# Kernel tuning notes

Hardware: AMD Instinct MI355X
Metric: run time of the kernel (lower is better)

## Reference

```python
import jax, jax.numpy as jnp
import numpy as np
from jax import lax

L, NFEAT, J, S = 200000, 128, 128, 16


def setup_inputs() -> dict:
    key = jax.random.key(0)
    ks = jax.random.split(key, 8)
    X = jax.random.normal(ks[0], (L, NFEAT), dtype=jnp.float32)
    perm_idx = jax.random.randint(ks[1], (L, 2, S), 0, L, dtype=jnp.int64)
    # torch.nn.Linear params: y = x @ W.T + b
    Wh = jax.random.normal(ks[2], (J, NFEAT), dtype=jnp.float32) * 0.05  # h1
    bh = jnp.zeros((J,), jnp.float32)
    Wg = jax.random.normal(ks[3], (J, 2 * J), dtype=jnp.float32) * 0.05  # g1
    bg = jnp.zeros((J,), jnp.float32)
    Wf = jax.random.normal(ks[4], (1, J), dtype=jnp.float32) * 0.05      # final1
    bf = jnp.zeros((1,), jnp.float32)
    return {"X": X, "perm_idx": perm_idx, "Wh": Wh, "bh": bh,
            "Wg": Wg, "bg": bg, "Wf": Wf, "bf": bf}


def reference(X, perm_idx, Wh, bh, Wg, bg, Wf, bf):
    # forward_recursive_vec with neighbor_subset_limit=2.
    # h(x) = relu(h1(x)) depends only on the row of X, so compute once and gather.
    Hmat = jax.nn.relu(X @ Wh.T + bh)                  # (L, J)
    Jdim = Wh.shape[0]
    Wg0, Wg1 = Wg[:, :Jdim], Wg[:, Jdim:]              # split of concat input
    n_samples = perm_idx.shape[-1]
    idxs = jnp.moveaxis(perm_idx, -1, 0)               # (S, L, 2)

    def body(acc, idx):
        # g(cat(h(X[perm0]), h(X[perm1]))) = relu(H[p0] @ Wg0.T + H[p1] @ Wg1.T + bg)
        h0 = Hmat[idx[:, 0]]                           # (L, J) irregular gather
        h1 = Hmat[idx[:, 1]]                           # (L, J) irregular gather
        g = jax.nn.relu(h0 @ Wg0.T + h1 @ Wg1.T + bg)
        return acc + g, None

    acc, _ = lax.scan(body, jnp.zeros_like(Hmat), idxs)
    E = jax.nn.relu(acc / n_samples)                   # E = relu(fk(X, 2))
    # temp = cat(h(X), E); E = g(temp)
    E = jax.nn.relu(Hmat @ Wg0.T + E @ Wg1.T + bg)
    # final(E): plain Linear(J,1), no sigmoid on this path
    return E @ Wf.T + bf                               # (L, 1)
```

## Files before the change

### kernel.cpp

```cpp
#include <hip/hip_runtime.h>

typedef unsigned short u16;
typedef unsigned char u8;
typedef unsigned int u32;
typedef __attribute__((ext_vector_type(8))) short short8;
typedef __attribute__((ext_vector_type(4))) short short4v;
typedef __attribute__((ext_vector_type(4))) float f32x4;
typedef __attribute__((ext_vector_type(2))) float f32x2;
typedef __attribute__((ext_vector_type(4))) u32 u32x4;

#define L_ROWS 200000
#define TM 64
#define LDP 136
#define NWH 16384
#define NWG 32768

__device__ __forceinline__ float b2f(u16 u) {
  union { u32 i; float f; } v; v.i = ((u32)u) << 16; return v.f;
}
__device__ __forceinline__ u16 f2b(float f) {
  union { float fv; u32 i; } v; v.fv = f;
  return (u16)((v.i + 0x7fffu + ((v.i >> 16) & 1u)) >> 16);
}
__device__ __forceinline__ u32 pk4_fp8(float f0, float f1, float f2, float f3) {
  u32 w = __builtin_amdgcn_cvt_pk_fp8_f32(f0, f1, 0, false);
  w = __builtin_amdgcn_cvt_pk_fp8_f32(f2, f3, w, true);
  return w;
}

__global__ __launch_bounds__(256) void kW(const float* __restrict__ Wh,
                                          const float* __restrict__ Wg,
                                          u16* __restrict__ WB) {
  int i = blockIdx.x * 256 + threadIdx.x;
  if (i < NWH) WB[i] = f2b(Wh[i]);
  else WB[i] = f2b(Wg[i - NWH]);
}

__global__ __launch_bounds__(256) void kA(const float* X,
                                          const float* bh,
                                          const u16* __restrict__ WB,
                                          u16* U0b, int strideB,
                                          u8* F0, u8* F1, int strideF) {
  __shared__ u16 tile[TM][LDP];
  const int b = blockIdx.x, t = threadIdx.x;
  const int wave = t >> 6, lane = t & 63;
  const int ln = lane & 15, quad = lane >> 4;
  const u16* WhB = WB;
  const u16* WgB = WB + NWH;

  {
    const float* src = X + (size_t)b * TM * 128;
#pragma unroll
    for (int i = 0; i < 8; i++) {
      int e = t * 4 + i * 1024;
      float4 v = *(const float4*)(src + e);
      u16 pk[4] = { f2b(v.x), f2b(v.y), f2b(v.z), f2b(v.w) };
      *(short4v*)&tile[e >> 7][e & 127] = *(const short4v*)pk;
    }
  }

  __syncthreads();

  f32x4 acc1[4][2] = {};
#pragma unroll
  for (int ks = 0; ks < 4; ks++) {
    short8 bf1[2];
#pragma unroll
    for (int nt = 0; nt < 2; nt++) {
      int n = wave * 32 + nt * 16 + ln;
      bf1[nt] = *(const short8*)(WhB + n * 128 + ks * 32 + quad * 8);
    }
    short8 af[4];
#pragma unroll
    for (int mt = 0; mt < 4; mt++) af[mt] = *(const short8*)&tile[mt * 16 + ln][ks * 32 + quad * 8];
#pragma unroll
    for (int mt = 0; mt < 4; mt++)
#pragma unroll
      for (int nt = 0; nt < 2; nt++)
        acc1[mt][nt] = __builtin_amdgcn_mfma_f32_16x16x32_bf16(af[mt], bf1[nt], acc1[mt][nt], 0, 0, 0);
  }

  __syncthreads();

#pragma unroll
  for (int nt = 0; nt < 2; nt++) {
    int n = wave * 32 + nt * 16 + ln;
    float bias = bh[n];
#pragma unroll
    for (int r = 0; r < 4; r++)
#pragma unroll
      for (int mt = 0; mt < 4; mt++)
        tile[mt * 16 + quad * 4 + r][n] = f2b(fmaxf(acc1[mt][nt][r] + bias, 0.f));
  }

  __syncthreads();

  f32x4 acc2[4][4] = {};
#pragma unroll
  for (int ks = 0; ks < 4; ks++) {
    short8 bf2[4];
#pragma unroll
    for (int nt = 0; nt < 4; nt++) {
      int n = wave * 64 + nt * 16 + ln;
      const u16* base = (n < 128) ? (WgB + n * 256) : (WgB + (n - 128) * 256 + 128);
      bf2[nt] = *(const short8*)(base + ks * 32 + quad * 8);
    }
    short8 af[4];
#pragma unroll
    for (int mt = 0; mt < 4; mt++) af[mt] = *(const short8*)&tile[mt * 16 + ln][ks * 32 + quad * 8];
#pragma unroll
    for (int mt = 0; mt < 4; mt++)
#pragma unroll
      for (int nt = 0; nt < 4; nt++)
        acc2[mt][nt] = __builtin_amdgcn_mfma_f32_16x16x32_bf16(af[mt], bf2[nt], acc2[mt][nt], 0, 0, 0);
  }

  __syncthreads();

  if (wave < 2) {
#pragma unroll
    for (int nt = 0; nt < 4; nt++) {
      int n = wave * 64 + nt * 16 + ln;
#pragma unroll
      for (int mt = 0; mt < 4; mt++)
#pragma unroll
        for (int r = 0; r < 4; r++)
          tile[mt * 16 + quad * 4 + r][n] = f2b(acc2[mt][nt][r]);
    }
  }
  __syncthreads();
  {
    const int rr = t >> 2, cs = (t & 3) * 32;
    const size_t row = (size_t)b * TM + rr;
    u16* dstB = U0b + row * strideB + cs;
    u8* dstF = F0 + row * strideF + cs;
    u32 wpk[8];
#pragma unroll
    for (int c = 0; c < 4; c++) {
      short8 v = *(const short8*)&tile[rr][cs + c * 8];
      *(short8*)(dstB + c * 8) = v;
      wpk[c * 2 + 0] = pk4_fp8(b2f((u16)v[0]), b2f((u16)v[1]), b2f((u16)v[2]), b2f((u16)v[3]));
      wpk[c * 2 + 1] = pk4_fp8(b2f((u16)v[4]), b2f((u16)v[5]), b2f((u16)v[6]), b2f((u16)v[7]));
    }
    *(u32x4*)dstF = u32x4{wpk[0], wpk[1], wpk[2], wpk[3]};
    *(u32x4*)(dstF + 16) = u32x4{wpk[4], wpk[5], wpk[6], wpk[7]};
  }
  __syncthreads();

  if (wave >= 2) {
#pragma unroll
    for (int nt = 0; nt < 4; nt++) {
      int n = wave * 64 + nt * 16 + ln - 128;
#pragma unroll
      for (int mt = 0; mt < 4; mt++)
#pragma unroll
        for (int r = 0; r < 4; r++)
          tile[mt * 16 + quad * 4 + r][n] = f2b(acc2[mt][nt][r]);
    }
  }
  __syncthreads();
  {
    const int rr = t >> 2, cs = (t & 3) * 32;
    const size_t row = (size_t)b * TM + rr;
    u8* dstF = F1 + row * strideF + cs;
    u32 wpk[8];
#pragma unroll
    for (int c = 0; c < 4; c++) {
      short8 v = *(const short8*)&tile[rr][cs + c * 8];
      wpk[c * 2 + 0] = pk4_fp8(b2f((u16)v[0]), b2f((u16)v[1]), b2f((u16)v[2]), b2f((u16)v[3]));
      wpk[c * 2 + 1] = pk4_fp8(b2f((u16)v[4]), b2f((u16)v[5]), b2f((u16)v[6]), b2f((u16)v[7]));
    }
    *(u32x4*)dstF = u32x4{wpk[0], wpk[1], wpk[2], wpk[3]};
    *(u32x4*)(dstF + 16) = u32x4{wpk[4], wpk[5], wpk[6], wpk[7]};
  }
}

__global__ __launch_bounds__(256) void kBC(const int* __restrict__ perm,
                                           const u16* __restrict__ U0b, int strideB,
                                           const u8* __restrict__ F0,
                                           const u8* __restrict__ F1, int strideF,
                                           const u16* __restrict__ WB,
                                           const float* __restrict__ bg,
                                           const float* __restrict__ Wf,
                                           const float* __restrict__ bfs,
                                           float* __restrict__ out) {
  __shared__ u16 Elds[TM][LDP];
  __shared__ float outacc[TM];
  const int b = blockIdx.x, t = threadIdx.x;
  const int wave = t >> 6, lane = t & 63;
  const int ln = lane & 15, quad = lane >> 4;
  const u16* WgB = WB + NWH;

  if (t < TM) outacc[t] = 0.f;

  const int r = t >> 2, cq = (t & 3) * 32;
  const size_t i = (size_t)b * TM + r;
  f32x2 bgp[16];
#pragma unroll
  for (int k = 0; k < 16; k++) bgp[k] = f32x2{bg[cq + 2 * k], bg[cq + 2 * k + 1]};

  f32x2 acc[16] = {};
  const int* pidx = perm + i * 32;
#pragma unroll 2
  for (int s = 0; s < 16; s++) {
    int i0 = pidx[s];
    int i1 = pidx[16 + s];
    const u32x4* p0 = (const u32x4*)(F0 + (size_t)i0 * strideF + cq);
    const u32x4* p1 = (const u32x4*)(F1 + (size_t)i1 * strideF + cq);
    u32x4 a0 = p0[0], a1 = p0[1];
    u32x4 c0 = p1[0], c1 = p1[1];
#pragma unroll
    for (int k = 0; k < 4; k++) {
      f32x2 va0 = __builtin_amdgcn_cvt_pk_f32_fp8(a0[k], false);
      f32x2 va1 = __builtin_amdgcn_cvt_pk_f32_fp8(a0[k], true);
      f32x2 vc0 = __builtin_amdgcn_cvt_pk_f32_fp8(c0[k], false);
      f32x2 vc1 = __builtin_amdgcn_cvt_pk_f32_fp8(c0[k], true);
      f32x2 s0 = va0 + vc0 + bgp[2 * k];
      f32x2 s1 = va1 + vc1 + bgp[2 * k + 1];
      acc[2 * k]     += __builtin_elementwise_max(s0, f32x2{0.f, 0.f});
      acc[2 * k + 1] += __builtin_elementwise_max(s1, f32x2{0.f, 0.f});
    }
#pragma unroll
    for (int k = 0; k < 4; k++) {
      f32x2 va0 = __builtin_amdgcn_cvt_pk_f32_fp8(a1[k], false);
      f32x2 va1 = __builtin_amdgcn_cvt_pk_f32_fp8(a1[k], true);
      f32x2 vc0 = __builtin_amdgcn_cvt_pk_f32_fp8(c1[k], false);
      f32x2 vc1 = __builtin_amdgcn_cvt_pk_f32_fp8(c1[k], true);
      f32x2 s0 = va0 + vc0 + bgp[8 + 2 * k];
      f32x2 s1 = va1 + vc1 + bgp[8 + 2 * k + 1];
      acc[8 + 2 * k]     += __builtin_elementwise_max(s0, f32x2{0.f, 0.f});
      acc[8 + 2 * k + 1] += __builtin_elementwise_max(s1, f32x2{0.f, 0.f});
    }
  }

#pragma unroll
  for (int j = 0; j < 4; j++) {
    u16 pk[8];
#pragma unroll
    for (int e = 0; e < 4; e++) {
      f32x2 v = acc[j * 4 + e];
      pk[e * 2]     = f2b(fmaxf(v[0] * 0.0625f, 0.f));
      pk[e * 2 + 1] = f2b(fmaxf(v[1] * 0.0625f, 0.f));
    }
    *(short8*)&Elds[r][cq + j * 8] = *(const short8*)pk;
  }

  __syncthreads();

  short8 bw[2][4];
#pragma unroll
  for (int nt = 0; nt < 2; nt++) {
    int n = wave * 32 + nt * 16 + ln;
#pragma unroll
    for (int ks = 0; ks < 4; ks++)
      bw[nt][ks] = *(const short8*)(WgB + n * 256 + 128 + ks * 32 + quad * 8);
  }

  f32x4 d[4][2] = {};
#pragma unroll
  for (int ks = 0; ks < 4; ks++) {
    short8 af[4];
#pragma unroll
    for (int mt = 0; mt < 4; mt++) af[mt] = *(const short8*)&Elds[mt * 16 + ln][ks * 32 + quad * 8];
#pragma unroll
    for (int mt = 0; mt < 4; mt++)
#pragma unroll
      for (int nt = 0; nt < 2; nt++)
        d[mt][nt] = __builtin_amdgcn_mfma_f32_16x16x32_bf16(af[mt], bw[nt][ks], d[mt][nt], 0, 0, 0);
  }

  float wfv[2], bgv2[2];
  int ncol[2];
#pragma unroll
  for (int nt = 0; nt < 2; nt++) {
    ncol[nt] = wave * 32 + nt * 16 + ln;
    wfv[nt] = Wf[ncol[nt]];
    bgv2[nt] = bg[ncol[nt]];
  }

#pragma unroll
  for (int mt = 0; mt < 4; mt++)
#pragma unroll
    for (int rr = 0; rr < 4; rr++) {
      int row = mt * 16 + quad * 4 + rr;
      size_t grow = (size_t)b * TM + row;
      float p = 0.f;
#pragma unroll
      for (int nt = 0; nt < 2; nt++) {
        float u0v = b2f(U0b[grow * strideB + ncol[nt]]);
        float e2 = fmaxf(d[mt][nt][rr] + u0v + bgv2[nt], 0.f);
        p += e2 * wfv[nt];
      }
      p += __shfl_xor(p, 1, 64);
      p += __shfl_xor(p, 2, 64);
      p += __shfl_xor(p, 4, 64);
      p += __shfl_xor(p, 8, 64);
      if (ln == 0) atomicAdd(&outacc[row], p);
    }

  __syncthreads();
  if (t < TM) out[(size_t)b * TM + t] = outacc[t] + bfs[0];
}

extern "C" void kernel_launch(void* const* d_in, const int* in_sizes, int n_in,
                              void* d_out, int out_size, void* d_ws, size_t ws_size,
                              hipStream_t stream) {
  const float* X  = (const float*)d_in[0];
  const int* perm = (const int*)d_in[1];
  const float* Wh = (const float*)d_in[2];
  const float* bh = (const float*)d_in[3];
  const float* Wg = (const float*)d_in[4];
  const float* bg = (const float*)d_in[5];
  const float* Wf = (const float*)d_in[6];
  const float* bf = (const float*)d_in[7];
  float* out = (float*)d_out;

  const size_t bfBytes = (size_t)L_ROWS * 128 * sizeof(u16);
  const size_t f8Bytes = (size_t)L_ROWS * 128;
  const size_t wBytes  = (size_t)(NWH + NWG) * sizeof(u16);

  u16* U0b; int strideB;
  u8 *F0, *F1; int strideF;
  u16* WB;
  if (ws_size >= bfBytes + 2 * f8Bytes + wBytes) {
    U0b = (u16*)d_ws;                    strideB = 128;
    F0 = (u8*)d_ws + bfBytes;            F1 = F0 + f8Bytes;   strideF = 128;
    WB = (u16*)(F1 + f8Bytes);
  } else {
    u8* base = (u8*)d_in[0];
    U0b = (u16*)base;                    strideB = 256;
    F0 = base + 256;                     F1 = base + 384;     strideF = 512;
    WB = (u16*)d_ws;
  }

  dim3 block(256);
  kW<<<dim3((NWH + NWG) / 256), block, 0, stream>>>(Wh, Wg, WB);
  kA<<<dim3(L_ROWS / TM), block, 0, stream>>>(X, bh, WB, U0b, strideB, F0, F1, strideF);
  kBC<<<dim3(L_ROWS / TM), block, 0, stream>>>(perm, U0b, strideB, F0, F1, strideF, WB, bg, Wf, bf, out);
}
```

Baseline: 378.4 us.

## Fold bias into F1 precompute and batch gather loads in sampling loop

The bias bg is now added to the second projection (F1) in kA before fp8 quantization, which removes the per-element bias add and its registers from the gather loop in kBC. kA uses two shared tiles so F0 and F1 are written in one pass with fewer barriers. kBC issues the gathers for four samples at once before converting, to get more memory requests in flight. It also drops the redundant relu after averaging non-negative sums. The costs are twice the shared memory in kA, higher register pressure in kBC, and a different fp8 rounding because the bias is quantized together with the projection.

```diff
diff --git a/kernel.cpp b/kernel.cpp
--- a/kernel.cpp
+++ b/kernel.cpp
@@ -38,10 +38,12 @@
 
 __global__ __launch_bounds__(256) void kA(const float* X,
                                           const float* bh,
+                                          const float* bg,
                                           const u16* __restrict__ WB,
                                           u16* U0b, int strideB,
                                           u8* F0, u8* F1, int strideF) {
-  __shared__ u16 tile[TM][LDP];
+  __shared__ u16 tileA[TM][LDP];
+  __shared__ u16 tileB[TM][LDP];
   const int b = blockIdx.x, t = threadIdx.x;
   const int wave = t >> 6, lane = t & 63;
   const int ln = lane & 15, quad = lane >> 4;
@@ -55,7 +57,7 @@
       int e = t * 4 + i * 1024;
       float4 v = *(const float4*)(src + e);
       u16 pk[4] = { f2b(v.x), f2b(v.y), f2b(v.z), f2b(v.w) };
-      *(short4v*)&tile[e >> 7][e & 127] = *(const short4v*)pk;
+      *(short4v*)&tileA[e >> 7][e & 127] = *(const short4v*)pk;
     }
   }
 
@@ -72,7 +74,7 @@
     }
     short8 af[4];
 #pragma unroll
-    for (int mt = 0; mt < 4; mt++) af[mt] = *(const short8*)&tile[mt * 16 + ln][ks * 32 + quad * 8];
+    for (int mt = 0; mt < 4; mt++) af[mt] = *(const short8*)&tileA[mt * 16 + ln][ks * 32 + quad * 8];
 #pragma unroll
     for (int mt = 0; mt < 4; mt++)
 #pragma unroll
@@ -90,7 +92,7 @@
     for (int r = 0; r < 4; r++)
 #pragma unroll
       for (int mt = 0; mt < 4; mt++)
-        tile[mt * 16 + quad * 4 + r][n] = f2b(fmaxf(acc1[mt][nt][r] + bias, 0.f));
+        tileA[mt * 16 + quad * 4 + r][n] = f2b(fmaxf(acc1[mt][nt][r] + bias, 0.f));
   }
 
   __syncthreads();
@@ -107,7 +109,7 @@
     }
     short8 af[4];
 #pragma unroll
-    for (int mt = 0; mt < 4; mt++) af[mt] = *(const short8*)&tile[mt * 16 + ln][ks * 32 + quad * 8];
+    for (int mt = 0; mt < 4; mt++) af[mt] = *(const short8*)&tileA[mt * 16 + ln][ks * 32 + quad * 8];
 #pragma unroll
     for (int mt = 0; mt < 4; mt++)
 #pragma unroll
@@ -125,53 +127,43 @@
       for (int mt = 0; mt < 4; mt++)
 #pragma unroll
         for (int r = 0; r < 4; r++)
-          tile[mt * 16 + quad * 4 + r][n] = f2b(acc2[mt][nt][r]);
-    }
-  }
-  __syncthreads();
+          tileA[mt * 16 + quad * 4 + r][n] = f2b(acc2[mt][nt][r]);
+    }
+  } else {
+#pragma unroll
+    for (int nt = 0; nt < 4; nt++) {
+      int n = wave * 64 + nt * 16 + ln - 128;
+      float bias = bg[n];
+#pragma unroll
+      for (int mt = 0; mt < 4; mt++)
+#pragma unroll
+        for (int r = 0; r < 4; r++)
+          tileB[mt * 16 + quad * 4 + r][n] = f2b(acc2[mt][nt][r] + bias);
+    }
+  }
+  __syncthreads();
+
   {
     const int rr = t >> 2, cs = (t & 3) * 32;
     const size_t row = (size_t)b * TM + rr;
     u16* dstB = U0b + row * strideB + cs;
-    u8* dstF = F0 + row * strideF + cs;
-    u32 wpk[8];
+    u8* dstF0 = F0 + row * strideF + cs;
+    u8* dstF1 = F1 + row * strideF + cs;
+    u32 w0[8], w1[8];
 #pragma unroll
     for (int c = 0; c < 4; c++) {
-      short8 v = *(const short8*)&tile[rr][cs + c * 8];
+      short8 v = *(const short8*)&tileA[rr][cs + c * 8];
       *(short8*)(dstB + c * 8) = v;
-      wpk[c * 2 + 0] = pk4_fp8(b2f((u16)v[0]), b2f((u16)v[1]), b2f((u16)v[2]), b2f((u16)v[3]));
-      wpk[c * 2 + 1] = pk4_fp8(b2f((u16)v[4]), b2f((u16)v[5]), b2f((u16)v[6]), b2f((u16)v[7]));
-    }
-    *(u32x4*)dstF = u32x4{wpk[0], wpk[1], wpk[2], wpk[3]};
-    *(u32x4*)(dstF + 16) = u32x4{wpk[4], wpk[5], wpk[6], wpk[7]};
-  }
-  __syncthreads();
-
-  if (wave >= 2) {
-#pragma unroll
-    for (int nt = 0; nt < 4; nt++) {
-      int n = wave * 64 + nt * 16 + ln - 128;
-#pragma unroll
-      for (int mt = 0; mt < 4; mt++)
-#pragma unroll
-        for (int r = 0; r < 4; r++)
-          tile[mt * 16 + quad * 4 + r][n] = f2b(acc2[mt][nt][r]);
-    }
-  }
-  __syncthreads();
-  {
-    const int rr = t >> 2, cs = (t & 3) * 32;
-    const size_t row = (size_t)b * TM + rr;
-    u8* dstF = F1 + row * strideF + cs;
-    u32 wpk[8];
-#pragma unroll
-    for (int c = 0; c < 4; c++) {
-      short8 v = *(const short8*)&tile[rr][cs + c * 8];
-      wpk[c * 2 + 0] = pk4_fp8(b2f((u16)v[0]), b2f((u16)v[1]), b2f((u16)v[2]), b2f((u16)v[3]));
-      wpk[c * 2 + 1] = pk4_fp8(b2f((u16)v[4]), b2f((u16)v[5]), b2f((u16)v[6]), b2f((u16)v[7]));
-    }
-    *(u32x4*)dstF = u32x4{wpk[0], wpk[1], wpk[2], wpk[3]};
-    *(u32x4*)(dstF + 16) = u32x4{wpk[4], wpk[5], wpk[6], wpk[7]};
+      w0[c * 2 + 0] = pk4_fp8(b2f((u16)v[0]), b2f((u16)v[1]), b2f((u16)v[2]), b2f((u16)v[3]));
+      w0[c * 2 + 1] = pk4_fp8(b2f((u16)v[4]), b2f((u16)v[5]), b2f((u16)v[6]), b2f((u16)v[7]));
+      short8 u = *(const short8*)&tileB[rr][cs + c * 8];
+      w1[c * 2 + 0] = pk4_fp8(b2f((u16)u[0]), b2f((u16)u[1]), b2f((u16)u[2]), b2f((u16)u[3]));
+      w1[c * 2 + 1] = pk4_fp8(b2f((u16)u[4]), b2f((u16)u[5]), b2f((u16)u[6]), b2f((u16)u[7]));
+    }
+    *(u32x4*)dstF0 = u32x4{w0[0], w0[1], w0[2], w0[3]};
+    *(u32x4*)(dstF0 + 16) = u32x4{w0[4], w0[5], w0[6], w0[7]};
+    *(u32x4*)dstF1 = u32x4{w1[0], w1[1], w1[2], w1[3]};
+    *(u32x4*)(dstF1 + 16) = u32x4{w1[4], w1[5], w1[6], w1[7]};
   }
 }
 
@@ -195,41 +187,37 @@
 
   const int r = t >> 2, cq = (t & 3) * 32;
   const size_t i = (size_t)b * TM + r;
-  f32x2 bgp[16];
-#pragma unroll
-  for (int k = 0; k < 16; k++) bgp[k] = f32x2{bg[cq + 2 * k], bg[cq + 2 * k + 1]};
+  const int* pidx = perm + i * 32;
 
   f32x2 acc[16] = {};
-  const int* pidx = perm + i * 32;
-#pragma unroll 2
-  for (int s = 0; s < 16; s++) {
-    int i0 = pidx[s];
-    int i1 = pidx[16 + s];
-    const u32x4* p0 = (const u32x4*)(F0 + (size_t)i0 * strideF + cq);
-    const u32x4* p1 = (const u32x4*)(F1 + (size_t)i1 * strideF + cq);
-    u32x4 a0 = p0[0], a1 = p0[1];
-    u32x4 c0 = p1[0], c1 = p1[1];
+  const f32x2 zero2 = {0.f, 0.f};
+#pragma unroll
+  for (int sb = 0; sb < 16; sb += 4) {
+    u32x4 A0[4], A1[4], C0[4], C1[4];
 #pragma unroll
     for (int k = 0; k < 4; k++) {
-      f32x2 va0 = __builtin_amdgcn_cvt_pk_f32_fp8(a0[k], false);
-      f32x2 va1 = __builtin_amdgcn_cvt_pk_f32_fp8(a0[k], true);
-      f32x2 vc0 = __builtin_amdgcn_cvt_pk_f32_fp8(c0[k], false);
-      f32x2 vc1 = __builtin_amdgcn_cvt_pk_f32_fp8(c0[k], true);
-      f32x2 s0 = va0 + vc0 + bgp[2 * k];
-      f32x2 s1 = va1 + vc1 + bgp[2 * k + 1];
-      acc[2 * k]     += __builtin_elementwise_max(s0, f32x2{0.f, 0.f});
-      acc[2 * k + 1] += __builtin_elementwise_max(s1, f32x2{0.f, 0.f});
+      const u8* r0 = F0 + (size_t)pidx[sb + k] * strideF + cq;
+      const u8* r1 = F1 + (size_t)pidx[16 + sb + k] * strideF + cq;
+      A0[k] = *(const u32x4*)r0; A1[k] = *(const u32x4*)(r0 + 16);
+      C0[k] = *(const u32x4*)r1; C1[k] = *(const u32x4*)(r1 + 16);
     }
 #pragma unroll
     for (int k = 0; k < 4; k++) {
-      f32x2 va0 = __builtin_amdgcn_cvt_pk_f32_fp8(a1[k], false);
-      f32x2 va1 = __builtin_amdgcn_cvt_pk_f32_fp8(a1[k], true);
-      f32x2 vc0 = __builtin_amdgcn_cvt_pk_f32_fp8(c1[k], false);
-      f32x2 vc1 = __builtin_amdgcn_cvt_pk_f32_fp8(c1[k], true);
-      f32x2 s0 = va0 + vc0 + bgp[8 + 2 * k];
-      f32x2 s1 = va1 + vc1 + bgp[8 + 2 * k + 1];
-      acc[8 + 2 * k]     += __builtin_elementwise_max(s0, f32x2{0.f, 0.f});
-      acc[8 + 2 * k + 1] += __builtin_elementwise_max(s1, f32x2{0.f, 0.f});
+#pragma unroll
+      for (int w = 0; w < 4; w++) {
+        f32x2 va0 = __builtin_amdgcn_cvt_pk_f32_fp8(A0[k][w], false);
+        f32x2 va1 = __builtin_amdgcn_cvt_pk_f32_fp8(A0[k][w], true);
+        f32x2 vc0 = __builtin_amdgcn_cvt_pk_f32_fp8(C0[k][w], false);
+        f32x2 vc1 = __builtin_amdgcn_cvt_pk_f32_fp8(C0[k][w], true);
+        acc[2 * w]     += __builtin_elementwise_max(va0 + vc0, zero2);
+        acc[2 * w + 1] += __builtin_elementwise_max(va1 + vc1, zero2);
+        f32x2 ua0 = __builtin_amdgcn_cvt_pk_f32_fp8(A1[k][w], false);
+        f32x2 ua1 = __builtin_amdgcn_cvt_pk_f32_fp8(A1[k][w], true);
+        f32x2 uc0 = __builtin_amdgcn_cvt_pk_f32_fp8(C1[k][w], false);
+        f32x2 uc1 = __builtin_amdgcn_cvt_pk_f32_fp8(C1[k][w], true);
+        acc[8 + 2 * w]     += __builtin_elementwise_max(ua0 + uc0, zero2);
+        acc[8 + 2 * w + 1] += __builtin_elementwise_max(ua1 + uc1, zero2);
+      }
     }
   }
 
@@ -239,8 +227,8 @@
 #pragma unroll
     for (int e = 0; e < 4; e++) {
       f32x2 v = acc[j * 4 + e];
-      pk[e * 2]     = f2b(fmaxf(v[0] * 0.0625f, 0.f));
-      pk[e * 2 + 1] = f2b(fmaxf(v[1] * 0.0625f, 0.f));
+      pk[e * 2]     = f2b(v[0] * 0.0625f);
+      pk[e * 2 + 1] = f2b(v[1] * 0.0625f);
     }
     *(short8*)&Elds[r][cq + j * 8] = *(const short8*)pk;
   }
@@ -335,6 +323,6 @@
 
   dim3 block(256);
   kW<<<dim3((NWH + NWG) / 256), block, 0, stream>>>(Wh, Wg, WB);
-  kA<<<dim3(L_ROWS / TM), block, 0, stream>>>(X, bh, WB, U0b, strideB, F0, F1, strideF);
+  kA<<<dim3(L_ROWS / TM), block, 0, stream>>>(X, bh, bg, WB, U0b, strideB, F0, F1, strideF);
   kBC<<<dim3(L_ROWS / TM), block, 0, stream>>>(perm, U0b, strideB, F0, F1, strideF, WB, bg, Wf, bf, out);
 }
```

Result: no change. 375.0 us (-0.9%).
